# Kernel tuning notes

Hardware: AMD Instinct MI355X
Metric: run time of the kernel (lower is better)

The kernel has to match this reference:

```python
import jax, jax.numpy as jnp
import numpy as np

B, N = 32, 512
NFEAT, NHID, NCLASS, NHEADS = 128, 64, 128, 8
WORK_D, SUB_D = 32, 32
H1, H2, OUT_D = 256, 256, 512
ALPHA = 0.2
NEG = -9e15


def setup_inputs() -> dict:
    key = jax.random.key(0)
    ks = jax.random.split(key, 16)
    return {
        "graph_inf": jax.random.normal(ks[0], (B, N, NFEAT), jnp.float32),
        "graph_matrix": jax.random.randint(ks[1], (B, N, N), 0, 2, jnp.int32),
        "masks": jnp.ones((B, N), jnp.float32),
        "node_order": jax.random.randint(ks[2], (B,), 0, N, jnp.int64),
        "work": jax.random.normal(ks[3], (B, WORK_D), jnp.float32),
        "subtask": jax.random.normal(ks[4], (B, SUB_D), jnp.float32),
        # GAT head params
        "W_heads": jax.random.normal(ks[5], (NHEADS, NFEAT, NHID), jnp.float32) * 0.1,
        "a_heads": jax.random.normal(ks[6], (NHEADS, 2 * NHID), jnp.float32) * 0.1,
        "W_out": jax.random.normal(ks[7], (NHID * NHEADS, NCLASS), jnp.float32) * 0.05,
        "a_out": jax.random.normal(ks[8], (2 * NCLASS,), jnp.float32) * 0.1,
        # MLP encoder params
        "fc1_w": jax.random.normal(ks[9], (NCLASS + WORK_D + SUB_D, H1), jnp.float32) * 0.07,
        "fc1_b": jnp.zeros((H1,), jnp.float32),
        "fc2_w": jax.random.normal(ks[10], (H1, H2), jnp.float32) * 0.06,
        "fc2_b": jnp.zeros((H2,), jnp.float32),
        "fc3_w": jax.random.normal(ks[11], (H2, OUT_D), jnp.float32) * 0.06,
        "fc3_b": jnp.zeros((OUT_D,), jnp.float32),
    }


def _gat_layer(Wh, a1, a2, adj, masks):
    # Wh: [B,N,F]; additive GAT score e_ij = leakyrelu(a1.Wh_i + a2.Wh_j)
    s1 = Wh @ a1  # [B,N]
    s2 = Wh @ a2  # [B,N]
    e = jax.nn.leaky_relu(s1[:, :, None] + s2[:, None, :], ALPHA)  # [B,N,N]
    att = jax.nn.softmax(jnp.where(adj > 0, e, NEG), axis=2)
    h_prime = jnp.einsum('bnm,bmf->bnf', att, Wh)
    return h_prime * masks[:, :, None]


def reference(graph_inf, graph_matrix, masks, node_order, work, subtask,
              W_heads, a_heads, W_out, a_out,
              fc1_w, fc1_b, fc2_w, fc2_b, fc3_w, fc3_b):
    adj = graph_matrix
    # multi-head GAT layer (concat=True -> ELU)
    def head(Wk, ak):
        Wh = jnp.einsum('bnf,fo->bno', graph_inf, Wk)
        return jax.nn.elu(_gat_layer(Wh, ak[:NHID], ak[NHID:], adj, masks))
    xh = jax.vmap(head)(W_heads, a_heads)  # [H,B,N,NHID]
    x = jnp.transpose(xh, (1, 2, 0, 3)).reshape(B, N, NHEADS * NHID)
    # output GAT layer (concat=False)
    Wh = jnp.einsum('bnf,fo->bno', x, W_out)
    x = _gat_layer(Wh, a_out[:NCLASS], a_out[NCLASS:], adj, masks)
    x = x * masks[:, :, None]
    # select subtask node per batch element
    selected = x[jnp.arange(B), node_order]  # [B,NCLASS]
    inf = jnp.concatenate([selected, work, subtask], axis=1)
    h = jax.nn.relu(inf @ fc1_w + fc1_b)
    h = jax.nn.relu(h @ fc2_w + fc2_b)
    out = h @ fc3_w + fc3_b
    return jax.nn.softmax(out, axis=-1)
```

## Files before the change

kernel.cpp:

```cpp
#include <hip/hip_runtime.h>

typedef unsigned short u16;
typedef unsigned int u32;
typedef unsigned long long u64;

typedef __bf16 bf16x8 __attribute__((ext_vector_type(8)));
typedef float f32x4 __attribute__((ext_vector_type(4)));

#define LOG2E 1.44269504088896340736f

__device__ __forceinline__ float b2f(u16 u) {
    u32 x = ((u32)u) << 16;
    return __builtin_bit_cast(float, x);
}
__device__ __forceinline__ u16 f2b(float f) {
    u32 u = __builtin_bit_cast(u32, f);
    u32 r = (u + 0x7fffu + ((u >> 16) & 1u)) >> 16;
    return (u16)r;
}
__device__ __forceinline__ float ld(const void* p, int i, bool bf) {
    return bf ? b2f(((const u16*)p)[i]) : ((const float*)p)[i];
}
__device__ __forceinline__ bool detect_bf16(const void* masks) {
    return ((const u16*)masks)[0] != 0;
}
__device__ __forceinline__ f32x4 mfma16(bf16x8 a, bf16x8 b, f32x4 c) {
    return __builtin_amdgcn_mfma_f32_16x16x32_bf16(a, b, c, 0, 0, 0);
}

__device__ __attribute__((aligned(256))) u32  g_adjm[16384 * 16];
__device__ __attribute__((aligned(256))) u16  g_BT1[512 * 128];
__device__ __attribute__((aligned(256))) u16  g_BT2[128 * 512];
__device__ __attribute__((aligned(256))) u16  g_Xc[32 * 512 * 128];
__device__ __attribute__((aligned(256))) u16  g_Wh1[512 * 16384];
__device__ __attribute__((aligned(256))) u16  g_xb[16384 * 512];
__device__ __attribute__((aligned(256))) u16  g_Wh2[16384 * 128];
__device__ __attribute__((aligned(256))) float g_s1a[131072];
__device__ __attribute__((aligned(256))) float g_s2a[131072];
__device__ __attribute__((aligned(256))) float g_s1b[16384];
__device__ __attribute__((aligned(256))) float g_s2b[16384];
__device__ __attribute__((aligned(256))) u16  g_fc1T[256 * 192];
__device__ __attribute__((aligned(256))) u16  g_fc2T[256 * 256];
__device__ __attribute__((aligned(256))) u16  g_fc3T[512 * 256];
__device__ __attribute__((aligned(256))) u16  g_Ahi[32 * 192];
__device__ __attribute__((aligned(256))) u16  g_Alo[32 * 192];
__device__ __attribute__((aligned(256))) u16  g_H1hi[32 * 256];
__device__ __attribute__((aligned(256))) u16  g_H1lo[32 * 256];
__device__ __attribute__((aligned(256))) u16  g_H2hi[32 * 256];
__device__ __attribute__((aligned(256))) u16  g_H2lo[32 * 256];
__device__ __attribute__((aligned(256))) float g_logits[32 * 512];

__global__ __launch_bounds__(256) void prep_kernel(
    const int* __restrict__ adj, const void* __restrict__ Whd,
    const void* __restrict__ Wo, const void* __restrict__ Xin,
    const void* __restrict__ fc1w, const void* __restrict__ fc2w,
    const void* __restrict__ fc3w, const void* __restrict__ masks)
{
    const bool bf = detect_bf16(masks);
    const int blk = blockIdx.x;
    const int tid = threadIdx.x;
    if (blk < 1024) {
        int id = blk * 256 + tid;
        int row = id >> 4, w = id & 15;
        const int4* p = (const int4*)(adj + row * 512 + w * 32);
        int4 v[8];
        #pragma unroll
        for (int s = 0; s < 8; ++s) v[s] = p[s];
        u32 word = 0;
        #pragma unroll
        for (int s = 0; s < 8; ++s) {
            u32 nib = (v[s].x > 0 ? 1u : 0u) | (v[s].y > 0 ? 2u : 0u) |
                      (v[s].z > 0 ? 4u : 0u) | (v[s].w > 0 ? 8u : 0u);
            word |= nib << (4 * s);
        }
        g_adjm[id] = word;
    } else if (blk < 1028) {
        int base = (blk - 1024) * 16384;
        for (int e = base + tid; e < base + 16384; e += 256) {
            int n = e >> 7, k = e & 127;
            g_BT1[e] = f2b(ld(Whd, (n >> 6) * 8192 + k * 64 + (n & 63), bf));
        }
    } else if (blk < 1032) {
        int base = (blk - 1028) * 16384;
        for (int e = base + tid; e < base + 16384; e += 256) {
            int n = e >> 9, k = e & 511;
            g_BT2[e] = f2b(ld(Wo, k * 128 + n, bf));
        }
    } else if (blk < 1288) {
        if (!bf) {
            int base = (blk - 1032) * 8192;
            for (int e = base + tid; e < base + 8192; e += 256)
                g_Xc[e] = f2b(((const float*)Xin)[e]);
        }
    } else if (blk < 1294) {
        int base = (blk - 1288) * 8192;
        for (int e = base + tid; e < base + 8192; e += 256) {
            int n = e / 192, k = e - n * 192;
            g_fc1T[e] = f2b(ld(fc1w, k * 256 + n, bf));
        }
    } else if (blk < 1302) {
        int base = (blk - 1294) * 8192;
        for (int e = base + tid; e < base + 8192; e += 256) {
            int n = e >> 8, k = e & 255;
            g_fc2T[e] = f2b(ld(fc2w, k * 256 + n, bf));
        }
    } else {
        int base = (blk - 1302) * 8192;
        for (int e = base + tid; e < base + 8192; e += 256) {
            int n = e >> 8, k = e & 255;
            g_fc3T[e] = f2b(ld(fc3w, k * 512 + n, bf));
        }
    }
}

__global__ __launch_bounds__(256, 2) void gemm1_kernel(
    const void* __restrict__ Xin, const void* __restrict__ a_heads,
    const void* __restrict__ masks)
{
    __shared__ __attribute__((aligned(16))) u16 Asl[128 * 72];
    __shared__ __attribute__((aligned(16))) u16 Bsl[128 * 72];
    const bool bf = detect_bf16(masks);
    const u16* Bsrc = bf ? (const u16*)Xin : g_Xc;
    const int tid = threadIdx.x;
    const int wave = tid >> 6, lane = tid & 63;
    const int wr = wave >> 1, wc = wave & 1;
    const int c = lane & 15, q = lane >> 4;
    const int tm = blockIdx.x * 128, tn = blockIdx.y * 128;
    const int srow = tid >> 1, sh = (tid & 1) * 32;
    f32x4 acc[4][4] = {};
    for (int kc = 0; kc < 128; kc += 64) {
        __syncthreads();
        const u16* Ag = g_BT1 + (tm + srow) * 128 + kc + sh;
        const u16* Bg = Bsrc + (tn + srow) * 128 + kc + sh;
        #pragma unroll
        for (int s = 0; s < 4; ++s) {
            *(uint4*)&Asl[srow * 72 + sh + 8 * s] = *(const uint4*)(Ag + 8 * s);
            *(uint4*)&Bsl[srow * 72 + sh + 8 * s] = *(const uint4*)(Bg + 8 * s);
        }
        __syncthreads();
        #pragma unroll
        for (int kt = 0; kt < 2; ++kt) {
            bf16x8 af[4], bfr[4];
            #pragma unroll
            for (int rt = 0; rt < 4; ++rt)
                af[rt] = *(const bf16x8*)&Asl[(wr * 64 + rt * 16 + c) * 72 + kt * 32 + q * 8];
            #pragma unroll
            for (int ct = 0; ct < 4; ++ct)
                bfr[ct] = *(const bf16x8*)&Bsl[(wc * 64 + ct * 16 + c) * 72 + kt * 32 + q * 8];
            #pragma unroll
            for (int rt = 0; rt < 4; ++rt)
                #pragma unroll
                for (int ct = 0; ct < 4; ++ct)
                    acc[rt][ct] = mfma16(af[rt], bfr[ct], acc[rt][ct]);
        }
    }
    #pragma unroll
    for (int rt = 0; rt < 4; ++rt)
        #pragma unroll
        for (int ct = 0; ct < 4; ++ct)
            #pragma unroll
            for (int i = 0; i < 4; ++i) {
                int r = tm + wr * 64 + rt * 16 + q * 4 + i;
                int col = tn + wc * 64 + ct * 16 + c;
                g_Wh1[r * 16384 + col] = f2b(acc[rt][ct][i]);
            }
    const int hh = blockIdx.x * 2 + wr;
    const int b = tn >> 9;
    const int nbase = (tn & 511) + wc * 64;
    float a1v[4][4], a2v[4][4];
    #pragma unroll
    for (int rt = 0; rt < 4; ++rt)
        #pragma unroll
        for (int i = 0; i < 4; ++i) {
            int o = rt * 16 + q * 4 + i;
            a1v[rt][i] = ld(a_heads, hh * 128 + o, bf);
            a2v[rt][i] = ld(a_heads, hh * 128 + 64 + o, bf);
        }
    #pragma unroll
    for (int ct = 0; ct < 4; ++ct) {
        float p1 = 0.f, p2 = 0.f;
        #pragma unroll
        for (int rt = 0; rt < 4; ++rt)
            #pragma unroll
            for (int i = 0; i < 4; ++i) {
                p1 += acc[rt][ct][i] * a1v[rt][i];
                p2 += acc[rt][ct][i] * a2v[rt][i];
            }
        p1 += __shfl_xor(p1, 16); p1 += __shfl_xor(p1, 32);
        p2 += __shfl_xor(p2, 16); p2 += __shfl_xor(p2, 32);
        if (lane < 16) {
            int n = nbase + ct * 16 + lane;
            g_s1a[(b * 8 + hh) * 512 + n] = p1 * LOG2E;
            g_s2a[(b * 8 + hh) * 512 + n] = p2 * LOG2E;
        }
    }
}

__global__ __launch_bounds__(512, 1) void att1_kernel(const void* __restrict__ masks)
{
    __shared__ __attribute__((aligned(16))) u16 WhL[64 * 520];
    __shared__ float E2s[512];
    __shared__ float E2ps[512];

    const bool bf = detect_bf16(masks);
    const int tid = threadIdx.x;
    const int w = tid >> 6, lane = tid & 63;
    const int c = lane & 15, q = lane >> 4;
    const int h  = blockIdx.x & 7;
    const int b  = blockIdx.x >> 3;

    const u16* wt = g_Wh1 + (u32)(h * 64) * 16384 + b * 512;
    {
        int r = tid >> 3, seg = tid & 7;
        const u16* src = wt + r * 16384 + seg * 64;
        u16* dst = &WhL[r * 520 + seg * 64];
        *(uint4*)dst = *(const uint4*)src;
        *(uint4*)(dst + 8) = *(const uint4*)(src + 8);
        *(uint4*)(dst + 16) = *(const uint4*)(src + 16);
        *(uint4*)(dst + 24) = *(const uint4*)(src + 24);
        *(uint4*)(dst + 32) = *(const uint4*)(src + 32);
        *(uint4*)(dst + 40) = *(const uint4*)(src + 40);
        *(uint4*)(dst + 48) = *(const uint4*)(src + 48);
        *(uint4*)(dst + 56) = *(const uint4*)(src + 56);
        float s2v = g_s2a[(b * 8 + h) * 512 + tid];
        E2s[tid]  = exp2f(s2v);
        E2ps[tid] = exp2f(0.2f * s2v);
    }
    __syncthreads();

    const u32* adjb = g_adjm + b * 8192;

    const u32 bword = (c == 0) ? 0x3F803F80u : 0u;
    const uint4 bq = {bword, bword, bword, bword};
    const bf16x8 bone = __builtin_bit_cast(bf16x8, bq);

    float E1[4], E1p[4];
    #pragma unroll
    for (int g = 0; g < 4; ++g) {
        float s1v = g_s1a[(b * 8 + h) * 512 + w * 64 + g * 16 + c];
        E1[g]  = exp2f(s1v);
        E1p[g] = exp2f(0.2f * s1v);
    }

    f32x4 acc[4][4] = {};
    f32x4 acc1[4] = {};
    const u16* lbase = &WhL[c * 520 + q * 8];

    for (int kc = 0; kc < 4; ++kc) {
        union { uint4 v; u32 a[4]; } wq[4];
        #pragma unroll
        for (int g = 0; g < 4; ++g)
            wq[g].v = *(const uint4*)(adjb + (w * 64 + g * 16 + c) * 16 + kc * 4);
        #pragma unroll
        for (int tl = 0; tl < 4; ++tl) {
            const int jb = kc * 128 + tl * 32 + q * 8;
            union { float4 v[2]; float f[8]; } e2r, e2pr;
            e2r.v[0]  = *(const float4*)&E2s[jb];
            e2r.v[1]  = *(const float4*)&E2s[jb + 4];
            e2pr.v[0] = *(const float4*)&E2ps[jb];
            e2pr.v[1] = *(const float4*)&E2ps[jb + 4];
            bf16x8 bfrag[4];
            #pragma unroll
            for (int nt = 0; nt < 4; ++nt)
                bfrag[nt] = *(const bf16x8*)(lbase + nt * 16 * 520 + kc * 128 + tl * 32);
            #pragma unroll
            for (int g = 0; g < 4; ++g) {
                u32 wbits = wq[g].a[tl] >> (q * 8);
                u32 pk[4];
                #pragma unroll
                for (int pi = 0; pi < 4; ++pi) {
                    float z0 = fmaxf(E1[g] * e2r.f[2 * pi],     E1p[g] * e2pr.f[2 * pi]);
                    float z1 = fmaxf(E1[g] * e2r.f[2 * pi + 1], E1p[g] * e2pr.f[2 * pi + 1]);
                    z0 = ((wbits >> (2 * pi)) & 1u) ? z0 : 0.f;
                    z1 = ((wbits >> (2 * pi + 1)) & 1u) ? z1 : 0.f;
                    pk[pi] = __builtin_amdgcn_perm(__builtin_bit_cast(u32, z1),
                                                   __builtin_bit_cast(u32, z0),
                                                   0x07060302u);
                }
                uint4 pkv = {pk[0], pk[1], pk[2], pk[3]};
                bf16x8 pv = __builtin_bit_cast(bf16x8, pkv);
                acc1[g] = mfma16(pv, bone, acc1[g]);
                #pragma unroll
                for (int nt = 0; nt < 4; ++nt)
                    acc[g][nt] = mfma16(pv, bfrag[nt], acc[g][nt]);
            }
        }
    }
    #pragma unroll
    for (int g = 0; g < 4; ++g) {
        const int R = w * 64 + g * 16;
        #pragma unroll
        for (int i = 0; i < 4; ++i) {
            float lr = __shfl(acc1[g][i], (lane & 48));
            float invr = (lr == 0.f) ? (1.f / 512.f) : (1.f / lr);
            const int row = R + q * 4 + i;
            float mk = ld(masks, b * 512 + row, bf);
            #pragma unroll
            for (int nt = 0; nt < 4; ++nt) {
                float v = acc[g][nt][i] * invr * mk;
                float o = v > 0.f ? v : (__expf(v) - 1.f);
                g_xb[(b * 512 + row) * 512 + h * 64 + nt * 16 + c] = f2b(o);
            }
        }
    }
}

__global__ __launch_bounds__(256, 2) void gemm2_kernel(
    const void* __restrict__ a_out, const void* __restrict__ masks)
{
    __shared__ __attribute__((aligned(16))) u16 Asl[64 * 72];
    __shared__ __attribute__((aligned(16))) u16 Bsl[128 * 72];
    const int tid = threadIdx.x;
    const int w = tid >> 6, lane = tid & 63;
    const int c = lane & 15, q = lane >> 4;
    const int tm = blockIdx.x * 64;
    const int rowA = tid >> 2, shA = (tid & 3) * 16;
    const int rowB = tid >> 1, shB = (tid & 1) * 32;
    f32x4 acc[8] = {};
    for (int kc = 0; kc < 512; kc += 64) {
        __syncthreads();
        const u16* Ag = g_xb + (tm + rowA) * 512 + kc + shA;
        *(uint4*)&Asl[rowA * 72 + shA] = *(const uint4*)Ag;
        *(uint4*)&Asl[rowA * 72 + shA + 8] = *(const uint4*)(Ag + 8);
        const u16* Bg = g_BT2 + rowB * 512 + kc + shB;
        #pragma unroll
        for (int s = 0; s < 4; ++s)
            *(uint4*)&Bsl[rowB * 72 + shB + 8 * s] = *(const uint4*)(Bg + 8 * s);
        __syncthreads();
        #pragma unroll
        for (int kt = 0; kt < 2; ++kt) {
            bf16x8 av = *(const bf16x8*)&Asl[(w * 16 + c) * 72 + kt * 32 + q * 8];
            #pragma unroll
            for (int ct = 0; ct < 8; ++ct) {
                bf16x8 bv = *(const bf16x8*)&Bsl[(ct * 16 + c) * 72 + kt * 32 + q * 8];
                acc[ct] = mfma16(av, bv, acc[ct]);
            }
        }
    }
    const bool bf = detect_bf16(masks);
    float a1v[8], a2v[8];
    #pragma unroll
    for (int ct = 0; ct < 8; ++ct) {
        a1v[ct] = ld(a_out, ct * 16 + c, bf);
        a2v[ct] = ld(a_out, 128 + ct * 16 + c, bf);
    }
    #pragma unroll
    for (int i = 0; i < 4; ++i) {
        float p1 = 0.f, p2 = 0.f;
        #pragma unroll
        for (int ct = 0; ct < 8; ++ct) {
            p1 += acc[ct][i] * a1v[ct];
            p2 += acc[ct][i] * a2v[ct];
        }
        #pragma unroll
        for (int off = 1; off < 16; off <<= 1) {
            p1 += __shfl_xor(p1, off);
            p2 += __shfl_xor(p2, off);
        }
        if (c == 0) {
            int m = tm + w * 16 + q * 4 + i;
            g_s1b[m] = p1 * LOG2E;
            g_s2b[m] = p2 * LOG2E;
        }
    }
    #pragma unroll
    for (int ct = 0; ct < 8; ++ct)
        #pragma unroll
        for (int i = 0; i < 4; ++i) {
            int m = tm + w * 16 + q * 4 + i;
            g_Wh2[m * 128 + ct * 16 + c] = f2b(acc[ct][i]);
        }
}

__global__ __launch_bounds__(256) void fin_att(
    const void* __restrict__ masks, const int* __restrict__ node_order,
    const void* __restrict__ workv, const void* __restrict__ subtaskv)
{
    __shared__ float att[512];
    __shared__ float parts[16][128];
    __shared__ float redl[4];

    const bool bf = detect_bf16(masks);
    const int b = blockIdx.x, t = threadIdx.x;
    const int lane = t & 63, wv = t >> 6;
    const int istar = node_order[b];

    const float s1v = g_s1b[b * 512 + istar];
    const u32* arow = g_adjm + (b * 512 + istar) * 16;
    float ssum = 0.f;
    #pragma unroll
    for (int rep = 0; rep < 2; ++rep) {
        int j = t + rep * 256;
        float e = s1v + g_s2b[b * 512 + j];
        e = fmaxf(e, 0.2f * e);
        float ex = ((arow[j >> 5] >> (j & 31)) & 1u) ? exp2f(e) : 0.f;
        att[j] = ex;
        ssum += ex;
    }
    for (int off = 1; off < 64; off <<= 1) ssum += __shfl_xor(ssum, off);
    if (lane == 0) redl[wv] = ssum;
    __syncthreads();
    float tot = redl[0] + redl[1] + redl[2] + redl[3];
    bool uni = (tot == 0.f);
    float inv = uni ? (1.f / 512.f) : (1.f / tot);

    const int og = t & 15, jg = t >> 4;
    float acc[8] = {};
    const u16* base = g_Wh2 + (b * 512 + jg * 32) * 128 + og * 8;
    #pragma unroll 8
    for (int j0 = 0; j0 < 32; ++j0) {
        float wgt = uni ? 1.f : att[jg * 32 + j0];
        union { u16 u[8]; uint4 v; } z;
        z.v = *(const uint4*)(base + j0 * 128);
        #pragma unroll
        for (int i = 0; i < 8; ++i) acc[i] += wgt * b2f(z.u[i]);
    }
    #pragma unroll
    for (int i = 0; i < 8; ++i) parts[jg][og * 8 + i] = acc[i];
    __syncthreads();
    float mk = ld(masks, b * 512 + istar, bf);
    if (t < 128) {
        float s = 0.f;
        #pragma unroll
        for (int jj = 0; jj < 16; ++jj) s += parts[jj][t];
        s *= inv * mk * mk;
        u16 hi = f2b(s);
        g_Ahi[b * 192 + t] = hi;
        g_Alo[b * 192 + t] = f2b(s - b2f(hi));
    } else if (t < 160) {
        g_Ahi[b * 192 + t] = bf ? ((const u16*)workv)[b * 32 + t - 128]
                                : f2b(((const float*)workv)[b * 32 + t - 128]);
        g_Alo[b * 192 + t] = 0;
    } else if (t < 192) {
        g_Ahi[b * 192 + t] = bf ? ((const u16*)subtaskv)[b * 32 + t - 160]
                                : f2b(((const float*)subtaskv)[b * 32 + t - 160]);
        g_Alo[b * 192 + t] = 0;
    }
}

template<int K, int NOUT, bool RELU>
__device__ __forceinline__ void mlp_body(
    const u16* __restrict__ Ahi, const u16* __restrict__ Alo,
    const u16* __restrict__ WT, const void* __restrict__ bias,
    u16* __restrict__ Ohi, u16* __restrict__ Olo, float* __restrict__ Of,
    const void* __restrict__ masks)
{
    const bool bf = detect_bf16(masks);
    const int t = threadIdx.x, w = t >> 6, lane = t & 63;
    const int c = lane & 15, q = lane >> 4;
    const int col = blockIdx.x * 64 + w * 16 + c;

    const u16* wp  = WT + col * K + q * 8;
    const u16* ahp = Ahi + c * K + q * 8;
    const u16* alp = Alo + c * K + q * 8;

    f32x4 acc0 = {}, acc1 = {};
    #pragma unroll
    for (int kt = 0; kt < K / 32; ++kt) {
        bf16x8 bw  = *(const bf16x8*)(wp + kt * 32);
        bf16x8 ah0 = *(const bf16x8*)(ahp + kt * 32);
        bf16x8 al0 = *(const bf16x8*)(alp + kt * 32);
        bf16x8 ah1 = *(const bf16x8*)(ahp + 16 * K + kt * 32);
        bf16x8 al1 = *(const bf16x8*)(alp + 16 * K + kt * 32);
        acc0 = mfma16(ah0, bw, acc0);
        acc0 = mfma16(al0, bw, acc0);
        acc1 = mfma16(ah1, bw, acc1);
        acc1 = mfma16(al1, bw, acc1);
    }
    float bs = ld(bias, col, bf);
    #pragma unroll
    for (int mt = 0; mt < 2; ++mt) {
        f32x4 a = mt ? acc1 : acc0;
        #pragma unroll
        for (int i = 0; i < 4; ++i) {
            int m = mt * 16 + q * 4 + i;
            float v = a[i] + bs;
            if (RELU) {
                v = fmaxf(v, 0.f);
                u16 hi = f2b(v);
                Ohi[m * NOUT + col] = hi;
                Olo[m * NOUT + col] = f2b(v - b2f(hi));
            } else {
                Of[m * NOUT + col] = v;
            }
        }
    }
}

__global__ __launch_bounds__(256) void mlp1_kernel(const void* bias, const void* masks) {
    mlp_body<192, 256, true>(g_Ahi, g_Alo, g_fc1T, bias, g_H1hi, g_H1lo, nullptr, masks);
}
__global__ __launch_bounds__(256) void mlp2_kernel(const void* bias, const void* masks) {
    mlp_body<256, 256, true>(g_H1hi, g_H1lo, g_fc2T, bias, g_H2hi, g_H2lo, nullptr, masks);
}
__global__ __launch_bounds__(256) void mlp3_kernel(const void* bias, const void* masks) {
    mlp_body<256, 512, false>(g_H2hi, g_H2lo, g_fc3T, bias, nullptr, nullptr, g_logits, masks);
}

__global__ __launch_bounds__(64) void softmax_kernel(
    const void* __restrict__ masks, void* __restrict__ out)
{
    const bool bf = detect_bf16(masks);
    const int row = blockIdx.x, lane = threadIdx.x;
    const float* lp = g_logits + row * 512 + lane * 8;
    float v[8];
    *(float4*)&v[0] = *(const float4*)lp;
    *(float4*)&v[4] = *(const float4*)(lp + 4);
    float mx = v[0];
    #pragma unroll
    for (int i = 1; i < 8; ++i) mx = fmaxf(mx, v[i]);
    for (int off = 1; off < 64; off <<= 1) mx = fmaxf(mx, __shfl_xor(mx, off));
    float e[8];
    float s = 0.f;
    #pragma unroll
    for (int i = 0; i < 8; ++i) { e[i] = __expf(v[i] - mx); s += e[i]; }
    for (int off = 1; off < 64; off <<= 1) s += __shfl_xor(s, off);
    float inv = 1.f / s;
    if (bf) {
        u16* o = (u16*)out + row * 512 + lane * 8;
        #pragma unroll
        for (int i = 0; i < 8; ++i) o[i] = f2b(e[i] * inv);
    } else {
        float* o = (float*)out + row * 512 + lane * 8;
        #pragma unroll
        for (int i = 0; i < 8; ++i) o[i] = e[i] * inv;
    }
}

extern "C" void kernel_launch(void* const* d_in, const int* in_sizes, int n_in,
                              void* d_out, int out_size, void* d_ws, size_t ws_size,
                              hipStream_t stream)
{
    const void* graph_inf    = d_in[0];
    const int*  graph_matrix = (const int*)d_in[1];
    const void* masks        = d_in[2];
    const int*  node_order   = (const int*)d_in[3];
    const void* work         = d_in[4];
    const void* subtask      = d_in[5];
    const void* W_heads      = d_in[6];
    const void* a_heads      = d_in[7];
    const void* W_out        = d_in[8];
    const void* a_out        = d_in[9];
    const void* fc1w         = d_in[10];
    const void* fc1b         = d_in[11];
    const void* fc2w         = d_in[12];
    const void* fc2b         = d_in[13];
    const void* fc3w         = d_in[14];
    const void* fc3b         = d_in[15];

    prep_kernel<<<dim3(1318), dim3(256), 0, stream>>>(graph_matrix, W_heads, W_out, graph_inf,
                                                      fc1w, fc2w, fc3w, masks);
    gemm1_kernel<<<dim3(4, 128), dim3(256), 0, stream>>>(graph_inf, a_heads, masks);
    att1_kernel<<<dim3(256), dim3(512), 0, stream>>>(masks);
    gemm2_kernel<<<dim3(256), dim3(256), 0, stream>>>(a_out, masks);
    fin_att<<<dim3(32), dim3(256), 0, stream>>>(masks, node_order, work, subtask);
    mlp1_kernel<<<dim3(4), dim3(256), 0, stream>>>(fc1b, masks);
    mlp2_kernel<<<dim3(4), dim3(256), 0, stream>>>(fc2b, masks);
    mlp3_kernel<<<dim3(8), dim3(256), 0, stream>>>(fc3b, masks);
    softmax_kernel<<<dim3(32), dim3(64), 0, stream>>>(masks, d_out);
}
```

Before: 192.6 us.

## Fuse head projection GEMM into first GAT attention kernel

Merges the per-head projection GEMM and the score dot-products into the attention kernel. Each block computes its head's 64xN Wh tile directly into shared memory and reduces the partial s1/s2 scores in LDS. This removes a kernel launch and the global write and read-back of the large Wh1 and score buffers. In exchange, LDS use per block rises sharply and the GEMM runs at only one block per CU before attention starts.

```diff
diff --git a/kernel.cpp b/kernel.cpp
--- a/kernel.cpp
+++ b/kernel.cpp
@@ -32,11 +32,8 @@
 __device__ __attribute__((aligned(256))) u16  g_BT1[512 * 128];
 __device__ __attribute__((aligned(256))) u16  g_BT2[128 * 512];
 __device__ __attribute__((aligned(256))) u16  g_Xc[32 * 512 * 128];
-__device__ __attribute__((aligned(256))) u16  g_Wh1[512 * 16384];
 __device__ __attribute__((aligned(256))) u16  g_xb[16384 * 512];
 __device__ __attribute__((aligned(256))) u16  g_Wh2[16384 * 128];
-__device__ __attribute__((aligned(256))) float g_s1a[131072];
-__device__ __attribute__((aligned(256))) float g_s2a[131072];
 __device__ __attribute__((aligned(256))) float g_s1b[16384];
 __device__ __attribute__((aligned(256))) float g_s2b[16384];
 __device__ __attribute__((aligned(256))) u16  g_fc1T[256 * 192];
@@ -113,92 +110,15 @@
     }
 }
 
-__global__ __launch_bounds__(256, 2) void gemm1_kernel(
+__global__ __launch_bounds__(512, 1) void gat1_kernel(
     const void* __restrict__ Xin, const void* __restrict__ a_heads,
     const void* __restrict__ masks)
 {
-    __shared__ __attribute__((aligned(16))) u16 Asl[128 * 72];
-    __shared__ __attribute__((aligned(16))) u16 Bsl[128 * 72];
-    const bool bf = detect_bf16(masks);
-    const u16* Bsrc = bf ? (const u16*)Xin : g_Xc;
-    const int tid = threadIdx.x;
-    const int wave = tid >> 6, lane = tid & 63;
-    const int wr = wave >> 1, wc = wave & 1;
-    const int c = lane & 15, q = lane >> 4;
-    const int tm = blockIdx.x * 128, tn = blockIdx.y * 128;
-    const int srow = tid >> 1, sh = (tid & 1) * 32;
-    f32x4 acc[4][4] = {};
-    for (int kc = 0; kc < 128; kc += 64) {
-        __syncthreads();
-        const u16* Ag = g_BT1 + (tm + srow) * 128 + kc + sh;
-        const u16* Bg = Bsrc + (tn + srow) * 128 + kc + sh;
-        #pragma unroll
-        for (int s = 0; s < 4; ++s) {
-            *(uint4*)&Asl[srow * 72 + sh + 8 * s] = *(const uint4*)(Ag + 8 * s);
-            *(uint4*)&Bsl[srow * 72 + sh + 8 * s] = *(const uint4*)(Bg + 8 * s);
-        }
-        __syncthreads();
-        #pragma unroll
-        for (int kt = 0; kt < 2; ++kt) {
-            bf16x8 af[4], bfr[4];
-            #pragma unroll
-            for (int rt = 0; rt < 4; ++rt)
-                af[rt] = *(const bf16x8*)&Asl[(wr * 64 + rt * 16 + c) * 72 + kt * 32 + q * 8];
-            #pragma unroll
-            for (int ct = 0; ct < 4; ++ct)
-                bfr[ct] = *(const bf16x8*)&Bsl[(wc * 64 + ct * 16 + c) * 72 + kt * 32 + q * 8];
-            #pragma unroll
-            for (int rt = 0; rt < 4; ++rt)
-                #pragma unroll
-                for (int ct = 0; ct < 4; ++ct)
-                    acc[rt][ct] = mfma16(af[rt], bfr[ct], acc[rt][ct]);
-        }
-    }
-    #pragma unroll
-    for (int rt = 0; rt < 4; ++rt)
-        #pragma unroll
-        for (int ct = 0; ct < 4; ++ct)
-            #pragma unroll
-            for (int i = 0; i < 4; ++i) {
-                int r = tm + wr * 64 + rt * 16 + q * 4 + i;
-                int col = tn + wc * 64 + ct * 16 + c;
-                g_Wh1[r * 16384 + col] = f2b(acc[rt][ct][i]);
-            }
-    const int hh = blockIdx.x * 2 + wr;
-    const int b = tn >> 9;
-    const int nbase = (tn & 511) + wc * 64;
-    float a1v[4][4], a2v[4][4];
-    #pragma unroll
-    for (int rt = 0; rt < 4; ++rt)
-        #pragma unroll
-        for (int i = 0; i < 4; ++i) {
-            int o = rt * 16 + q * 4 + i;
-            a1v[rt][i] = ld(a_heads, hh * 128 + o, bf);
-            a2v[rt][i] = ld(a_heads, hh * 128 + 64 + o, bf);
-        }
-    #pragma unroll
-    for (int ct = 0; ct < 4; ++ct) {
-        float p1 = 0.f, p2 = 0.f;
-        #pragma unroll
-        for (int rt = 0; rt < 4; ++rt)
-            #pragma unroll
-            for (int i = 0; i < 4; ++i) {
-                p1 += acc[rt][ct][i] * a1v[rt][i];
-                p2 += acc[rt][ct][i] * a2v[rt][i];
-            }
-        p1 += __shfl_xor(p1, 16); p1 += __shfl_xor(p1, 32);
-        p2 += __shfl_xor(p2, 16); p2 += __shfl_xor(p2, 32);
-        if (lane < 16) {
-            int n = nbase + ct * 16 + lane;
-            g_s1a[(b * 8 + hh) * 512 + n] = p1 * LOG2E;
-            g_s2a[(b * 8 + hh) * 512 + n] = p2 * LOG2E;
-        }
-    }
-}
-
-__global__ __launch_bounds__(512, 1) void att1_kernel(const void* __restrict__ masks)
-{
     __shared__ __attribute__((aligned(16))) u16 WhL[64 * 520];
+    __shared__ __attribute__((aligned(16))) u16 As[64 * 136];
+    __shared__ __attribute__((aligned(16))) u16 XcL[128 * 136];
+    __shared__ float s1p[4][512];
+    __shared__ float s2p[4][512];
     __shared__ float E2s[512];
     __shared__ float E2ps[512];
 
@@ -209,27 +129,78 @@
     const int h  = blockIdx.x & 7;
     const int b  = blockIdx.x >> 3;
 
-    const u16* wt = g_Wh1 + (u32)(h * 64) * 16384 + b * 512;
+    const u16* Bsrc = bf ? (const u16*)Xin : g_Xc;
+
     {
-        int r = tid >> 3, seg = tid & 7;
-        const u16* src = wt + r * 16384 + seg * 64;
-        u16* dst = &WhL[r * 520 + seg * 64];
-        *(uint4*)dst = *(const uint4*)src;
-        *(uint4*)(dst + 8) = *(const uint4*)(src + 8);
-        *(uint4*)(dst + 16) = *(const uint4*)(src + 16);
-        *(uint4*)(dst + 24) = *(const uint4*)(src + 24);
-        *(uint4*)(dst + 32) = *(const uint4*)(src + 32);
-        *(uint4*)(dst + 40) = *(const uint4*)(src + 40);
-        *(uint4*)(dst + 48) = *(const uint4*)(src + 48);
-        *(uint4*)(dst + 56) = *(const uint4*)(src + 56);
-        float s2v = g_s2a[(b * 8 + h) * 512 + tid];
-        E2s[tid]  = exp2f(s2v);
-        E2ps[tid] = exp2f(0.2f * s2v);
+        int r = tid >> 3, seg = (tid & 7) * 16;
+        const u16* src = g_BT1 + (h * 64 + r) * 128 + seg;
+        *(uint4*)&As[r * 136 + seg] = *(const uint4*)src;
+        *(uint4*)&As[r * 136 + seg + 8] = *(const uint4*)(src + 8);
+    }
+
+    const int wm = w & 3, wn = w >> 2;
+    float a1v[4], a2v[4];
+    #pragma unroll
+    for (int i = 0; i < 4; ++i) {
+        int o = wm * 16 + q * 4 + i;
+        a1v[i] = ld(a_heads, h * 128 + o, bf);
+        a2v[i] = ld(a_heads, h * 128 + 64 + o, bf);
+    }
+
+    for (int chunk = 0; chunk < 4; ++chunk) {
+        __syncthreads();
+        {
+            int r = tid >> 2, seg = (tid & 3) * 32;
+            const u16* src = Bsrc + (b * 512 + chunk * 128 + r) * 128 + seg;
+            u16* dst = &XcL[r * 136 + seg];
+            *(uint4*)dst = *(const uint4*)src;
+            *(uint4*)(dst + 8) = *(const uint4*)(src + 8);
+            *(uint4*)(dst + 16) = *(const uint4*)(src + 16);
+            *(uint4*)(dst + 24) = *(const uint4*)(src + 24);
+        }
+        __syncthreads();
+        f32x4 cacc[4] = {};
+        #pragma unroll
+        for (int kt = 0; kt < 4; ++kt) {
+            bf16x8 af = *(const bf16x8*)&As[(wm * 16 + c) * 136 + kt * 32 + q * 8];
+            #pragma unroll
+            for (int nt = 0; nt < 4; ++nt) {
+                bf16x8 bv = *(const bf16x8*)&XcL[(wn * 64 + nt * 16 + c) * 136 + kt * 32 + q * 8];
+                cacc[nt] = mfma16(af, bv, cacc[nt]);
+            }
+        }
+        #pragma unroll
+        for (int nt = 0; nt < 4; ++nt) {
+            const int ncol = chunk * 128 + wn * 64 + nt * 16 + c;
+            float p1 = 0.f, p2 = 0.f;
+            #pragma unroll
+            for (int i = 0; i < 4; ++i) {
+                float v = cacc[nt][i];
+                WhL[(wm * 16 + q * 4 + i) * 520 + ncol] = f2b(v);
+                p1 += v * a1v[i];
+                p2 += v * a2v[i];
+            }
+            p1 += __shfl_xor(p1, 16); p1 += __shfl_xor(p1, 32);
+            p2 += __shfl_xor(p2, 16); p2 += __shfl_xor(p2, 32);
+            if (lane < 16) {
+                int n = chunk * 128 + wn * 64 + nt * 16 + lane;
+                s1p[wm][n] = p1;
+                s2p[wm][n] = p2;
+            }
+        }
     }
     __syncthreads();
+    {
+        float s2v = (s2p[0][tid & 511] + s2p[1][tid & 511] +
+                     s2p[2][tid & 511] + s2p[3][tid & 511]) * LOG2E;
+        if (tid < 512) {
+            E2s[tid]  = exp2f(s2v);
+            E2ps[tid] = exp2f(0.2f * s2v);
+        }
+    }
+    __syncthreads();
 
     const u32* adjb = g_adjm + b * 8192;
-
     const u32 bword = (c == 0) ? 0x3F803F80u : 0u;
     const uint4 bq = {bword, bword, bword, bword};
     const bf16x8 bone = __builtin_bit_cast(bf16x8, bq);
@@ -237,7 +208,8 @@
     float E1[4], E1p[4];
     #pragma unroll
     for (int g = 0; g < 4; ++g) {
-        float s1v = g_s1a[(b * 8 + h) * 512 + w * 64 + g * 16 + c];
+        int r = w * 64 + g * 16 + c;
+        float s1v = (s1p[0][r] + s1p[1][r] + s1p[2][r] + s1p[3][r]) * LOG2E;
         E1[g]  = exp2f(s1v);
         E1p[g] = exp2f(0.2f * s1v);
     }
@@ -550,8 +522,7 @@
 
     prep_kernel<<<dim3(1318), dim3(256), 0, stream>>>(graph_matrix, W_heads, W_out, graph_inf,
                                                       fc1w, fc2w, fc3w, masks);
-    gemm1_kernel<<<dim3(4, 128), dim3(256), 0, stream>>>(graph_inf, a_heads, masks);
-    att1_kernel<<<dim3(256), dim3(512), 0, stream>>>(masks);
+    gat1_kernel<<<dim3(256), dim3(512), 0, stream>>>(graph_inf, a_heads, masks);
     gemm2_kernel<<<dim3(256), dim3(256), 0, stream>>>(a_out, masks);
     fin_att<<<dim3(32), dim3(256), 0, stream>>>(masks, node_order, work, subtask);
     mlp1_kernel<<<dim3(4), dim3(256), 0, stream>>>(fc1b, masks);
```

New measurement: 191.3 us. Within noise of the previous version (-0.7%).
